# Optimization experiments

Measured on AMD Instinct MI355X. Metric: run time of the kernel, lower is better.

The kernel has to match this reference:

```python
import jax, jax.numpy as jnp
import numpy as np

B = 1024      # number of subgraphs in the batch
S = 128       # nodes per subgraph (last node is the anchor)
N = B * S     # total nodes
E = 2_097_152 # total edges (avg degree 16)
F_IN = 300
F_OUT = 64


def setup_inputs() -> dict:
    key = jax.random.key(0)
    kx, kg, ks, kd, kw = jax.random.split(key, 5)
    in_feat = jax.random.normal(kx, (N, F_IN), dtype=jnp.float32)
    # edges constrained within subgraphs (batched DGL graph semantics)
    gid = jax.random.randint(kg, (E,), 0, B)
    src = (gid * S + jax.random.randint(ks, (E,), 0, S)).astype(jnp.int32)
    dst = (gid * S + jax.random.randint(kd, (E,), 0, S)).astype(jnp.int32)
    W = jax.random.normal(kw, (F_IN, F_OUT), dtype=jnp.float32) * 0.05
    b = jnp.zeros((F_OUT,), dtype=jnp.float32)
    prelu_a = jnp.float32(0.25)  # nn.PReLU default single parameter
    return {"in_feat": in_feat, "W": W, "b": b, "prelu_a": prelu_a,
            "src": src, "dst": dst}


def reference(in_feat, W, b, prelu_a, src, dst):
    ones = jnp.ones((E,), dtype=jnp.float32)
    deg_out = jnp.clip(jax.ops.segment_sum(ones, src, num_segments=N), 1.0)
    deg_in = jnp.clip(jax.ops.segment_sum(ones, dst, num_segments=N), 1.0)
    # GraphConv norm='both': weight first (in_feats > out_feats), then SpMM
    x = in_feat * jax.lax.rsqrt(deg_out)[:, None]
    h = x @ W                                   # [N, F_OUT]
    agg = jax.ops.segment_sum(h[src], dst, num_segments=N)
    h = agg * jax.lax.rsqrt(deg_in)[:, None] + b
    # PReLU
    h = jnp.where(h > 0, h, prelu_a * h)
    # ragged per-subgraph mean over all nodes except the last (anchor)
    node_idx = jnp.arange(N)
    seg = node_idx // S                          # subgraph id per node
    not_anchor = ((node_idx % S) != (S - 1)).astype(h.dtype)
    pool_sum = jax.ops.segment_sum(h * not_anchor[:, None], seg, num_segments=B)
    subgraph_pool_emb = pool_sum / jnp.float32(S - 1)
    anchor_out = h[(jnp.arange(B) + 1) * S - 1]  # last node of each subgraph
    return subgraph_pool_emb, anchor_out
```

## Files before the change

### kernel.cpp

```cpp
#include <hip/hip_runtime.h>
#include <hip/hip_bf16.h>

#define NNODES 131072
#define NEDGES 2097152
#define BSUB   1024
#define SSUB   128
#define FIN    300
#define FOUT   64
#define NCHUNK 256
#define CHEDGE 8192

typedef __attribute__((ext_vector_type(8))) short short8;
typedef __attribute__((ext_vector_type(8))) unsigned short ushort8;
typedef __attribute__((ext_vector_type(4))) float f32x4;

__device__ inline short f2bf(float f) {
    unsigned u = __float_as_uint(f);
    u = (u + 0x7FFFu + ((u >> 16) & 1u)) >> 16;
    return (short)u;
}
__device__ inline float bf2f(unsigned short b) {
    return __uint_as_float(((unsigned)b) << 16);
}

__global__ __launch_bounds__(256) void prep_w_kernel(const float* __restrict__ W,
                                                     short* __restrict__ wfrag,
                                                     int* __restrict__ gcnt) {
    int idx = blockIdx.x * 256 + threadIdx.x;
    if (idx < BSUB) gcnt[idx] = 0;
    if (idx >= 2560) return;
    int ct   = idx / 640;
    int rem  = idx % 640;
    int kt   = rem / 64;
    int lane = rem % 64;
    int col  = ct * 16 + (lane & 15);
    int kb   = kt * 32 + (lane >> 4) * 8;
#pragma unroll
    for (int e = 0; e < 8; ++e) {
        int k = kb + e;
        float v = (k < FIN) ? W[(size_t)k * FOUT + col] : 0.f;
        wfrag[(size_t)idx * 8 + e] = f2bf(v);
    }
}

__global__ __launch_bounds__(256) void bucket_kernel(const int* __restrict__ src,
                                                     const int* __restrict__ dst,
                                                     int* __restrict__ gcnt,
                                                     unsigned short* __restrict__ bkt) {
    __shared__ unsigned short epack[CHEDGE];
    __shared__ unsigned short eg[CHEDGE];
    __shared__ int hist[BSUB];
    const int t = threadIdx.x;
    for (int i = t; i < BSUB; i += 256) hist[i] = 0;
    __syncthreads();
    const int4* sp = (const int4*)(src + (size_t)blockIdx.x * CHEDGE);
    const int4* dp = (const int4*)(dst + (size_t)blockIdx.x * CHEDGE);
    for (int i = t; i < CHEDGE / 4; i += 256) {
        int4 s4 = sp[i], d4 = dp[i];
#pragma unroll
        for (int k = 0; k < 4; ++k) {
            int s = (k == 0) ? s4.x : (k == 1) ? s4.y : (k == 2) ? s4.z : s4.w;
            int d = (k == 0) ? d4.x : (k == 1) ? d4.y : (k == 2) ? d4.z : d4.w;
            int g = s >> 7;
            epack[i * 4 + k] = (unsigned short)(((s & 127) << 7) | (d & 127));
            eg[i * 4 + k] = (unsigned short)g;
            atomicAdd(&hist[g], 1);
        }
    }
    __syncthreads();
    for (int i = t; i < BSUB; i += 256) {
        int c = hist[i];
        hist[i] = c ? atomicAdd(&gcnt[i], c) : 0;
    }
    __syncthreads();
    for (int i = t; i < CHEDGE; i += 256) {
        int g = eg[i];
        int r = atomicAdd(&hist[g], 1);
        bkt[((size_t)g << 12) + r] = epack[i];
    }
}

__global__ __launch_bounds__(256) void gcn_fused_kernel(const float* __restrict__ x,
                                                        const short* __restrict__ wfrag,
                                                        const unsigned short* __restrict__ bkt,
                                                        const int* __restrict__ gcnt,
                                                        const float* __restrict__ bias,
                                                        const float* __restrict__ prelu,
                                                        float* __restrict__ out) {
    __shared__ unsigned short hl[SSUB][FOUT];
    __shared__ unsigned char  es[SSUB][64];
    __shared__ int   din[SSUB];
    __shared__ int   dout[SSUB];
    __shared__ float rout[SSUB];
    __shared__ float ps[4][FOUT];

    const int g = blockIdx.x;
    const int t = threadIdx.x;
    const int lane = t & 63;
    const int w = t >> 6;

    if (t < SSUB) { din[t] = 0; dout[t] = 0; }
    __syncthreads();

    const int cnt = gcnt[g];
    const unsigned short* eb = bkt + ((size_t)g << 12);
    for (int i = t; i < cnt; i += 256) {
        unsigned e = eb[i];
        int s = e >> 7, d = e & 127;
        int r = atomicAdd(&din[d], 1);
        es[d][r & 63] = (unsigned char)s;
        atomicAdd(&dout[s], 1);
    }

    f32x4 acc[2][4];
#pragma unroll
    for (int rt = 0; rt < 2; ++rt)
#pragma unroll
        for (int c = 0; c < 4; ++c) acc[rt][c] = (f32x4){0.f, 0.f, 0.f, 0.f};

    const int kgrp = lane >> 4;
#pragma unroll
    for (int rt = 0; rt < 2; ++rt) {
        const int arow = g * SSUB + w * 32 + rt * 16 + (lane & 15);
        const float* ap = x + (size_t)arow * FIN + kgrp * 8;
#pragma unroll
        for (int kt = 0; kt < 9; ++kt) {
            f32x4 lo = *(const f32x4*)(ap + kt * 32);
            f32x4 hi = *(const f32x4*)(ap + kt * 32 + 4);
            short8 afr;
            afr[0] = f2bf(lo[0]); afr[1] = f2bf(lo[1]);
            afr[2] = f2bf(lo[2]); afr[3] = f2bf(lo[3]);
            afr[4] = f2bf(hi[0]); afr[5] = f2bf(hi[1]);
            afr[6] = f2bf(hi[2]); afr[7] = f2bf(hi[3]);
#pragma unroll
            for (int ct = 0; ct < 4; ++ct) {
                short8 bfr = *(const short8*)(wfrag + ((size_t)(ct * 10 + kt) * 64 + lane) * 8);
                acc[rt][ct] = __builtin_amdgcn_mfma_f32_16x16x32_bf16(afr, bfr, acc[rt][ct], 0, 0, 0);
            }
        }
        {
            short8 afr;
#pragma unroll
            for (int e = 0; e < 8; ++e) {
                int k = 288 + kgrp * 8 + e;
                float v = (k < FIN) ? x[(size_t)arow * FIN + k] : 0.f;
                afr[e] = f2bf(v);
            }
#pragma unroll
            for (int ct = 0; ct < 4; ++ct) {
                short8 bfr = *(const short8*)(wfrag + ((size_t)(ct * 10 + 9) * 64 + lane) * 8);
                acc[rt][ct] = __builtin_amdgcn_mfma_f32_16x16x32_bf16(afr, bfr, acc[rt][ct], 0, 0, 0);
            }
        }
    }
    __syncthreads();

#pragma unroll
    for (int rt = 0; rt < 2; ++rt) {
        const int lrow = w * 32 + rt * 16 + (lane >> 4) * 4;
        const int colb = lane & 15;
#pragma unroll
        for (int ct = 0; ct < 4; ++ct)
#pragma unroll
            for (int r = 0; r < 4; ++r)
                hl[lrow + r][ct * 16 + colb] = (unsigned short)f2bf(acc[rt][ct][r]);
    }
    if (t < SSUB) rout[t] = rsqrtf((float)max(dout[t], 1));
    __syncthreads();

    const float bv = bias[lane];
    const float a = prelu[0];
    float pool = 0.f;
#pragma unroll 4
    for (int ii = 0; ii < 32; ++ii) {
        int d = w + 4 * ii;
        int cd = min(din[d], 64);
        float accv = 0.f;
        const unsigned* ew = (const unsigned*)&es[d][0];
        int nw = (cd + 3) >> 2;
        for (int p = 0; p < nw; ++p) {
            unsigned wd = ew[p];
            int rem = cd - p * 4;
#pragma unroll
            for (int b = 0; b < 4; ++b) {
                if (b < rem) {
                    int s = (wd >> (8 * b)) & 127;
                    accv += bf2f(hl[s][lane]) * rout[s];
                }
            }
        }
        float v = accv * rsqrtf((float)max(din[d], 1)) + bv;
        v = (v > 0.f) ? v : a * v;
        if (d == SSUB - 1)
            out[(size_t)(BSUB + g) * FOUT + lane] = v;
        else
            pool += v;
    }
    ps[w][lane] = pool;
    __syncthreads();
    if (w == 0) {
        float s = (ps[0][lane] + ps[1][lane]) + (ps[2][lane] + ps[3][lane]);
        out[(size_t)g * FOUT + lane] = s * (1.0f / 127.0f);
    }
}

extern "C" void kernel_launch(void* const* d_in, const int* in_sizes, int n_in,
                              void* d_out, int out_size, void* d_ws, size_t ws_size,
                              hipStream_t stream) {
    const float* in_feat = (const float*)d_in[0];
    const float* W       = (const float*)d_in[1];
    const float* bias    = (const float*)d_in[2];
    const float* prelu   = (const float*)d_in[3];
    const int*   src     = (const int*)d_in[4];
    const int*   dst     = (const int*)d_in[5];
    float* out = (float*)d_out;

    char* ws = (char*)d_ws;
    int*            gcnt  = (int*)(ws);
    short*          wfrag = (short*)(ws + 65536);
    unsigned short* bkt   = (unsigned short*)(ws + (1u << 20));

    hipLaunchKernelGGL(prep_w_kernel,   dim3(10),       dim3(256), 0, stream, W, wfrag, gcnt);
    hipLaunchKernelGGL(bucket_kernel,   dim3(NCHUNK),   dim3(256), 0, stream, src, dst, gcnt, bkt);
    hipLaunchKernelGGL(gcn_fused_kernel,dim3(BSUB),     dim3(256), 0, stream, in_feat, wfrag, bkt, gcnt, bias, prelu, out);
}
```

Baseline: 112.7 us.

## Split fused GCN kernel into separate GEMM and aggregation-pool kernels

Moves the dense X@W bf16 MFMA projection out of the per-subgraph fused kernel into its own kernel with 2048 blocks of 64 rows. The result goes to a bf16 global buffer, which the aggregation kernel then copies into LDS. This is meant to expose more parallelism and memory-level concurrency for the bandwidth-heavy read of in_feat, instead of 1024 blocks each doing GEMM plus edge work. The cost is an extra launch and a round trip of about 16 MB of intermediate through global memory. It also replaces the hand-written bf16 rounding with the library conversion.

```diff
diff --git a/kernel.cpp b/kernel.cpp
--- a/kernel.cpp
+++ b/kernel.cpp
@@ -14,10 +14,10 @@
 typedef __attribute__((ext_vector_type(8))) unsigned short ushort8;
 typedef __attribute__((ext_vector_type(4))) float f32x4;
 
-__device__ inline short f2bf(float f) {
-    unsigned u = __float_as_uint(f);
-    u = (u + 0x7FFFu + ((u >> 16) & 1u)) >> 16;
-    return (short)u;
+__device__ inline unsigned short f2bfbits(float f) {
+    union { __hip_bfloat16 h; unsigned short u; } cv;
+    cv.h = __float2bfloat16(f);
+    return cv.u;
 }
 __device__ inline float bf2f(unsigned short b) {
     return __uint_as_float(((unsigned)b) << 16);
@@ -39,7 +39,7 @@
     for (int e = 0; e < 8; ++e) {
         int k = kb + e;
         float v = (k < FIN) ? W[(size_t)k * FOUT + col] : 0.f;
-        wfrag[(size_t)idx * 8 + e] = f2bf(v);
+        wfrag[(size_t)idx * 8 + e] = (short)f2bfbits(v);
     }
 }
 
@@ -80,13 +80,64 @@
     }
 }
 
-__global__ __launch_bounds__(256) void gcn_fused_kernel(const float* __restrict__ x,
-                                                        const short* __restrict__ wfrag,
-                                                        const unsigned short* __restrict__ bkt,
-                                                        const int* __restrict__ gcnt,
-                                                        const float* __restrict__ bias,
-                                                        const float* __restrict__ prelu,
-                                                        float* __restrict__ out) {
+__global__ __launch_bounds__(256) void gemm_kernel(const float* __restrict__ x,
+                                                   const short* __restrict__ wfrag,
+                                                   unsigned short* __restrict__ hb) {
+    const int wave = threadIdx.x >> 6;
+    const int lane = threadIdx.x & 63;
+    const int rowbase = (blockIdx.x * 4 + wave) * 16;
+    const int arow = rowbase + (lane & 15);
+    const int kgrp = lane >> 4;
+
+    f32x4 acc[4];
+#pragma unroll
+    for (int c = 0; c < 4; ++c) acc[c] = (f32x4){0.f, 0.f, 0.f, 0.f};
+
+    const float* ap = x + (size_t)arow * FIN + kgrp * 8;
+#pragma unroll
+    for (int kt = 0; kt < 9; ++kt) {
+        f32x4 lo = *(const f32x4*)(ap + kt * 32);
+        f32x4 hi = *(const f32x4*)(ap + kt * 32 + 4);
+        short8 afr;
+        afr[0] = (short)f2bfbits(lo[0]); afr[1] = (short)f2bfbits(lo[1]);
+        afr[2] = (short)f2bfbits(lo[2]); afr[3] = (short)f2bfbits(lo[3]);
+        afr[4] = (short)f2bfbits(hi[0]); afr[5] = (short)f2bfbits(hi[1]);
+        afr[6] = (short)f2bfbits(hi[2]); afr[7] = (short)f2bfbits(hi[3]);
+#pragma unroll
+        for (int ct = 0; ct < 4; ++ct) {
+            short8 bfr = *(const short8*)(wfrag + ((size_t)(ct * 10 + kt) * 64 + lane) * 8);
+            acc[ct] = __builtin_amdgcn_mfma_f32_16x16x32_bf16(afr, bfr, acc[ct], 0, 0, 0);
+        }
+    }
+    {
+        short8 afr;
+#pragma unroll
+        for (int e = 0; e < 8; ++e) {
+            int k = 288 + kgrp * 8 + e;
+            float v = (k < FIN) ? x[(size_t)arow * FIN + k] : 0.f;
+            afr[e] = (short)f2bfbits(v);
+        }
+#pragma unroll
+        for (int ct = 0; ct < 4; ++ct) {
+            short8 bfr = *(const short8*)(wfrag + ((size_t)(ct * 10 + 9) * 64 + lane) * 8);
+            acc[ct] = __builtin_amdgcn_mfma_f32_16x16x32_bf16(afr, bfr, acc[ct], 0, 0, 0);
+        }
+    }
+    const int orow = rowbase + (lane >> 4) * 4;
+    const int colb = lane & 15;
+#pragma unroll
+    for (int ct = 0; ct < 4; ++ct)
+#pragma unroll
+        for (int r = 0; r < 4; ++r)
+            hb[(size_t)(orow + r) * FOUT + ct * 16 + colb] = f2bfbits(acc[ct][r]);
+}
+
+__global__ __launch_bounds__(256) void agg_pool_kernel(const unsigned short* __restrict__ hb,
+                                                       const unsigned short* __restrict__ bkt,
+                                                       const int* __restrict__ gcnt,
+                                                       const float* __restrict__ bias,
+                                                       const float* __restrict__ prelu,
+                                                       float* __restrict__ out) {
     __shared__ unsigned short hl[SSUB][FOUT];
     __shared__ unsigned char  es[SSUB][64];
     __shared__ int   din[SSUB];
@@ -99,11 +150,17 @@
     const int lane = t & 63;
     const int w = t >> 6;
 
+    {
+        const ushort8* hsrc = (const ushort8*)(hb + (size_t)g * SSUB * FOUT);
+        ushort8* hdst = (ushort8*)&hl[0][0];
+        for (int i = t; i < 1024; i += 256) hdst[i] = hsrc[i];
+    }
     if (t < SSUB) { din[t] = 0; dout[t] = 0; }
     __syncthreads();
 
     const int cnt = gcnt[g];
     const unsigned short* eb = bkt + ((size_t)g << 12);
+
     for (int i = t; i < cnt; i += 256) {
         unsigned e = eb[i];
         int s = e >> 7, d = e & 127;
@@ -111,60 +168,7 @@
         es[d][r & 63] = (unsigned char)s;
         atomicAdd(&dout[s], 1);
     }
-
-    f32x4 acc[2][4];
-#pragma unroll
-    for (int rt = 0; rt < 2; ++rt)
-#pragma unroll
-        for (int c = 0; c < 4; ++c) acc[rt][c] = (f32x4){0.f, 0.f, 0.f, 0.f};
-
-    const int kgrp = lane >> 4;
-#pragma unroll
-    for (int rt = 0; rt < 2; ++rt) {
-        const int arow = g * SSUB + w * 32 + rt * 16 + (lane & 15);
-        const float* ap = x + (size_t)arow * FIN + kgrp * 8;
-#pragma unroll
-        for (int kt = 0; kt < 9; ++kt) {
-            f32x4 lo = *(const f32x4*)(ap + kt * 32);
-            f32x4 hi = *(const f32x4*)(ap + kt * 32 + 4);
-            short8 afr;
-            afr[0] = f2bf(lo[0]); afr[1] = f2bf(lo[1]);
-            afr[2] = f2bf(lo[2]); afr[3] = f2bf(lo[3]);
-            afr[4] = f2bf(hi[0]); afr[5] = f2bf(hi[1]);
-            afr[6] = f2bf(hi[2]); afr[7] = f2bf(hi[3]);
-#pragma unroll
-            for (int ct = 0; ct < 4; ++ct) {
-                short8 bfr = *(const short8*)(wfrag + ((size_t)(ct * 10 + kt) * 64 + lane) * 8);
-                acc[rt][ct] = __builtin_amdgcn_mfma_f32_16x16x32_bf16(afr, bfr, acc[rt][ct], 0, 0, 0);
-            }
-        }
-        {
-            short8 afr;
-#pragma unroll
-            for (int e = 0; e < 8; ++e) {
-                int k = 288 + kgrp * 8 + e;
-                float v = (k < FIN) ? x[(size_t)arow * FIN + k] : 0.f;
-                afr[e] = f2bf(v);
-            }
-#pragma unroll
-            for (int ct = 0; ct < 4; ++ct) {
-                short8 bfr = *(const short8*)(wfrag + ((size_t)(ct * 10 + 9) * 64 + lane) * 8);
-                acc[rt][ct] = __builtin_amdgcn_mfma_f32_16x16x32_bf16(afr, bfr, acc[rt][ct], 0, 0, 0);
-            }
-        }
-    }
-    __syncthreads();
-
-#pragma unroll
-    for (int rt = 0; rt < 2; ++rt) {
-        const int lrow = w * 32 + rt * 16 + (lane >> 4) * 4;
-        const int colb = lane & 15;
-#pragma unroll
-        for (int ct = 0; ct < 4; ++ct)
-#pragma unroll
-            for (int r = 0; r < 4; ++r)
-                hl[lrow + r][ct * 16 + colb] = (unsigned short)f2bf(acc[rt][ct][r]);
-    }
+    __syncthreads();
     if (t < SSUB) rout[t] = rsqrtf((float)max(dout[t], 1));
     __syncthreads();
 
@@ -219,8 +223,10 @@
     int*            gcnt  = (int*)(ws);
     short*          wfrag = (short*)(ws + 65536);
     unsigned short* bkt   = (unsigned short*)(ws + (1u << 20));
-
-    hipLaunchKernelGGL(prep_w_kernel,   dim3(10),       dim3(256), 0, stream, W, wfrag, gcnt);
-    hipLaunchKernelGGL(bucket_kernel,   dim3(NCHUNK),   dim3(256), 0, stream, src, dst, gcnt, bkt);
-    hipLaunchKernelGGL(gcn_fused_kernel,dim3(BSUB),     dim3(256), 0, stream, in_feat, wfrag, bkt, gcnt, bias, prelu, out);
-}
+    unsigned short* hb    = (unsigned short*)(ws + (16u << 20));
+
+    hipLaunchKernelGGL(prep_w_kernel,   dim3(10),        dim3(256), 0, stream, W, wfrag, gcnt);
+    hipLaunchKernelGGL(bucket_kernel,   dim3(NCHUNK),    dim3(256), 0, stream, src, dst, gcnt, bkt);
+    hipLaunchKernelGGL(gemm_kernel,     dim3(NNODES/64), dim3(256), 0, stream, in_feat, wfrag, hb);
+    hipLaunchKernelGGL(agg_pool_kernel, dim3(BSUB),      dim3(256), 0, stream, hb, bkt, gcnt, bias, prelu, out);
+}
```

After: 121.0 us. 7.4% more time.
